# Optimization experiments

Hardware: AMD Instinct MI355X
Metric: run time of the kernel (lower is better)

## Reference

```python
import jax, jax.numpy as jnp
import numpy as np


def _scattering(image, mags, phases):
    # image: [B,S,S] real; mags/phases: [J,L,S,S] real (Fourier-domain Morlet filters)
    J = mags.shape[0]
    psi = (mags * jnp.exp(1j * phases)).astype(jnp.complex64)        # [J,L,S,S]
    xf = jnp.fft.fft2(image)                                          # [B,S,S] complex64
    # first-order: modulus of wavelet convolutions, all scales/orientations at once
    u1 = jnp.abs(jnp.fft.ifft2(xf[:, None, None] * psi[None]))        # [B,J,L,S,S]
    s0 = image.mean(axis=(-2, -1))                                    # [B]
    s1 = u1.mean(axis=(2, 3, 4))                                      # [B,J] (orientation-averaged)
    # second-order: only j2 > j1 (the nan-filtered entries in the original)
    s2_parts = []
    for j1 in range(J - 1):  # structural loop over scales, not data dims
        u1f = jnp.fft.fft2(u1[:, j1].astype(jnp.complex64))           # [B,L1,S,S]
        psi2 = psi[j1 + 1:]                                           # [J2,L2,S,S]
        v = jnp.abs(jnp.fft.ifft2(u1f[:, :, None, None] * psi2[None, None]))  # [B,L1,J2,L2,S,S]
        s2_parts.append(v.mean(axis=(1, 3, 4, 5)))                    # [B,J2]
    s2 = jnp.concatenate(s2_parts, axis=1)                            # [B, J*(J-1)/2]
    return s0, s1, s2


def setup_inputs() -> dict:
    key = jax.random.key(0)
    ks = jax.random.split(key, 8)
    B, S, J, L = 64, 128, 6, 4
    return {
        "image_batch": jax.random.normal(ks[0], (B, S, S), dtype=jnp.float32),
        "mags": jax.random.uniform(ks[1], (J, L, S, S), dtype=jnp.float32),
        "phases": jax.random.normal(ks[2], (J, L, S, S), dtype=jnp.float32),
        "w1": jax.random.normal(ks[3], (22, 16), dtype=jnp.float32) * 0.1,
        "b1": jnp.zeros((16,), dtype=jnp.float32),
        "w2": jax.random.normal(ks[4], (16, 16), dtype=jnp.float32) * 0.1,
        "b2": jnp.zeros((16,), dtype=jnp.float32),
        "w3": jax.random.normal(ks[5], (16, 1), dtype=jnp.float32) * 0.1,
        "b3": jnp.zeros((1,), dtype=jnp.float32),
    }


def reference(image_batch, mags, phases, w1, b1, w2, b2, w3, b3):
    s0, s1, s2 = _scattering(image_batch, mags, phases)
    x = jnp.concatenate([s0[:, None], s1, s2], axis=1)                # [B,22]
    x = jax.nn.relu(x @ w1 + b1)
    x = jax.nn.relu(x @ w2 + b2)
    x = jax.nn.sigmoid(x @ w3 + b3)
    return jnp.squeeze(x, axis=1)                                     # [B]
```

## Files before the change

kernel.cpp:

```cpp
#include <hip/hip_runtime.h>
#include <math.h>


#define SDIM 128
#define PLANE 16384
#define PITCH 129
#define NT 1024
#define TWO_PI 6.28318530717958647692f
#define PSIH_SCALE 16.0f

typedef _Float16 h2 __attribute__((ext_vector_type(2)));

constexpr float W16R[8] = {1.f, 0.9238795325f, 0.7071067812f, 0.3826834324f,
                           0.f, -0.3826834324f, -0.7071067812f, -0.9238795325f};
constexpr float W16I[8] = {0.f, -0.3826834324f, -0.7071067812f, -0.9238795325f,
                           -1.f, -0.9238795325f, -0.7071067812f, -0.3826834324f};

__device__ __forceinline__ float fast_sqrtf(float x) { return __builtin_amdgcn_sqrtf(x); }

__device__ __forceinline__ unsigned packbf(float re, float im) {
  const unsigned r = __float_as_uint(re) + 0x8000u;
  const unsigned i = __float_as_uint(im) + 0x8000u;
  return __builtin_amdgcn_perm(r, i, 0x07060302u);
}
__device__ __forceinline__ void unpackbf(unsigned u, float& re, float& im) {
  re = __uint_as_float(u & 0xFFFF0000u);
  im = __uint_as_float(u << 16);
}

union UHU { unsigned u; h2 h; };
__device__ __forceinline__ h2 u2h(unsigned u) { UHU x; x.u = u; return x.h; }
__device__ __forceinline__ unsigned h2u(h2 h) { UHU x; x.h = h; return x.u; }
__device__ __forceinline__ h2 bch2(float f) { const _Float16 h = (_Float16)f; h2 v = {h, h}; return v; }
__device__ __forceinline__ h2 mkh2(float a, float b) { h2 v = {(_Float16)a, (_Float16)b}; return v; }

__device__ __forceinline__ void stC(float2* s, int idx, float re, float im) { s[idx] = make_float2(re, im); }
__device__ __forceinline__ void ldC(const float2* s, int idx, float& re, float& im) { const float2 v = s[idx]; re = v.x; im = v.y; }
__device__ __forceinline__ void stC(unsigned* s, int idx, float re, float im) { s[idx] = packbf(re, im); }
__device__ __forceinline__ void ldC(const unsigned* s, int idx, float& re, float& im) { unpackbf(s[idx], re, im); }

__device__ __forceinline__ void load_tw(const float2* __restrict__ twg, int g,
                                        float* twr, float* twi) {
#pragma unroll
  for (int k = 1; k < 16; ++k) {
    const float2 w = twg[16 * g + k];
    twr[k] = __uint_as_float(__builtin_amdgcn_readfirstlane(__float_as_uint(w.x)));
    twi[k] = __uint_as_float(__builtin_amdgcn_readfirstlane(__float_as_uint(w.y)));
  }
}
__device__ __forceinline__ void load_twh(const uint2* __restrict__ twgh, int g,
                                         unsigned* twru, unsigned* twiu) {
#pragma unroll
  for (int k = 1; k < 16; ++k) {
    const uint2 w = twgh[16 * g + k];
    twru[k] = (unsigned)__builtin_amdgcn_readfirstlane((int)w.x);
    twiu[k] = (unsigned)__builtin_amdgcn_readfirstlane((int)w.y);
  }
}

template<bool INV>
__device__ __forceinline__ void bfly(float& ar, float& ai, float& br, float& bi, const int idx) {
  float tr, ti;
  if (idx == 0) { tr = br; ti = bi; }
  else if (idx == 4) {
    if (INV) { tr = -bi; ti = br; } else { tr = bi; ti = -br; }
  } else {
    const float wr = W16R[idx];
    const float wi = INV ? -W16I[idx] : W16I[idx];
    tr = br * wr - bi * wi;
    ti = br * wi + bi * wr;
  }
  br = ar - tr; bi = ai - ti;
  ar = ar + tr; ai = ai + ti;
}

#define CSWAP(re, im, a, b) { float _t = re[a]; re[a]=re[b]; re[b]=_t; _t = im[a]; im[a]=im[b]; im[b]=_t; }

template<bool INV>
__device__ __forceinline__ void dft16(float* re, float* im) {
  CSWAP(re, im, 1, 8) CSWAP(re, im, 2, 4) CSWAP(re, im, 3, 12)
  CSWAP(re, im, 5, 10) CSWAP(re, im, 7, 14) CSWAP(re, im, 11, 13)
#pragma unroll
  for (int ls = 1; ls <= 4; ++ls) {
    const int len = 1 << ls, half = len >> 1, tstep = 16 >> ls;
#pragma unroll
    for (int blk = 0; blk < 16; blk += len)
#pragma unroll
      for (int j = 0; j < half; ++j)
        bfly<INV>(re[blk + j], im[blk + j], re[blk + j + half], im[blk + j + half], j * tstep);
  }
}

template<bool INV>
__device__ __forceinline__ void dft8(float* re, float* im) {
  CSWAP(re, im, 1, 4) CSWAP(re, im, 3, 6)
#pragma unroll
  for (int ls = 1; ls <= 3; ++ls) {
    const int len = 1 << ls, half = len >> 1, tstep = 8 >> ls;
#pragma unroll
    for (int blk = 0; blk < 8; blk += len)
#pragma unroll
      for (int j = 0; j < half; ++j)
        bfly<INV>(re[blk + j], im[blk + j], re[blk + j + half], im[blk + j + half], j * tstep * 2);
  }
}

__device__ __forceinline__ void twmul_fwd(float* R, float* I, const float* twr, const float* twi) {
#pragma unroll
  for (int k = 1; k < 16; ++k) {
    const float r = R[k] * twr[k] - I[k] * twi[k];
    I[k] = R[k] * twi[k] + I[k] * twr[k]; R[k] = r;
  }
}
__device__ __forceinline__ void twmul_inv(float* R, float* I, const float* twr, const float* twi) {
#pragma unroll
  for (int k = 1; k < 16; ++k) {
    const float r = R[k] * twr[k] + I[k] * twi[k];
    I[k] = I[k] * twr[k] - R[k] * twi[k]; R[k] = r;
  }
}

template<typename S>
__device__ __forceinline__ void fwd_fft2(float* R, float* I, S* sC,
                                         int g, int q, const float* twr, const float* twi) {
  const int rb = q * PITCH;
  dft16<false>(R, I);
  twmul_fwd(R, I, twr, twi);
  __syncthreads();
#pragma unroll
  for (int k = 0; k < 16; ++k) stC(sC, rb + 8 * k + g, R[k], I[k]);
  __syncthreads();
#pragma unroll
  for (int t = 0; t < 8; ++t) {
    ldC(sC, rb + 16 * g + t, R[t], I[t]);
    ldC(sC, rb + 16 * g + 8 + t, R[8 + t], I[8 + t]);
  }
  dft8<false>(R, I); dft8<false>(R + 8, I + 8);
#pragma unroll
  for (int k2 = 0; k2 < 8; ++k2) {
    stC(sC, rb + 16 * g + k2, R[k2], I[k2]);
    stC(sC, rb + 16 * g + 8 + k2, R[8 + k2], I[8 + k2]);
  }
  __syncthreads();
#pragma unroll
  for (int m = 0; m < 16; ++m) ldC(sC, (g + 8 * m) * PITCH + q, R[m], I[m]);
  dft16<false>(R, I);
  twmul_fwd(R, I, twr, twi);
#pragma unroll
  for (int k = 0; k < 16; ++k) stC(sC, (8 * k + g) * PITCH + q, R[k], I[k]);
  __syncthreads();
#pragma unroll
  for (int u = 0; u < 8; ++u) {
    const int bp = (16 * g + 2 * u) * PITCH + q;
    ldC(sC, bp, R[2 * u], I[2 * u]);
    ldC(sC, bp + PITCH, R[2 * u + 1], I[2 * u + 1]);
  }
  dft8<false>(R, I); dft8<false>(R + 8, I + 8);
}

template<bool FIRST, typename S>
__device__ __forceinline__ void inv_fft2(float* R, float* I, S* sC,
                                         int g, int q, const float* twr, const float* twi) {
  const int rb = q * PITCH;
  dft8<true>(R, I); dft8<true>(R + 8, I + 8);
  if constexpr (!FIRST) __syncthreads();
#pragma unroll
  for (int t = 0; t < 16; ++t) stC(sC, rb + 16 * g + t, R[t], I[t]);
  __syncthreads();
#pragma unroll
  for (int k = 0; k < 16; ++k) ldC(sC, rb + 8 * k + g, R[k], I[k]);
  twmul_inv(R, I, twr, twi);
  dft16<true>(R, I);
#pragma unroll
  for (int m = 0; m < 16; ++m) stC(sC, rb + g + 8 * m, R[m], I[m]);
  __syncthreads();
#pragma unroll
  for (int u = 0; u < 8; ++u) {
    const int bp = (16 * g + 2 * u) * PITCH + q;
    ldC(sC, bp, R[2 * u], I[2 * u]);
    ldC(sC, bp + PITCH, R[2 * u + 1], I[2 * u + 1]);
  }
  dft8<true>(R, I); dft8<true>(R + 8, I + 8);
#pragma unroll
  for (int u = 0; u < 8; ++u) {
    const int bp = (16 * g + 2 * u) * PITCH + q;
    stC(sC, bp, R[2 * u], I[2 * u]);
    stC(sC, bp + PITCH, R[2 * u + 1], I[2 * u + 1]);
  }
  __syncthreads();
#pragma unroll
  for (int k = 0; k < 16; ++k) ldC(sC, (8 * k + g) * PITCH + q, R[k], I[k]);
  twmul_inv(R, I, twr, twi);
  dft16<true>(R, I);
}

__device__ __forceinline__ void bfly_h_inv(h2& ar, h2& ai, h2& br, h2& bi, const int idx) {
  h2 tr, ti;
  if (idx == 0) { tr = br; ti = bi; }
  else if (idx == 4) { tr = -bi; ti = br; }
  else {
    const h2 wr = bch2(W16R[idx]);
    const h2 wi = bch2(-W16I[idx]);
    tr = br * wr - bi * wi;
    ti = br * wi + bi * wr;
  }
  br = ar - tr; bi = ai - ti;
  ar = ar + tr; ai = ai + ti;
}

#define HSWAP(re, im, a, b) { h2 _t = re[a]; re[a]=re[b]; re[b]=_t; _t = im[a]; im[a]=im[b]; im[b]=_t; }

__device__ __forceinline__ void dft16h(h2* re, h2* im) {
  HSWAP(re, im, 1, 8) HSWAP(re, im, 2, 4) HSWAP(re, im, 3, 12)
  HSWAP(re, im, 5, 10) HSWAP(re, im, 7, 14) HSWAP(re, im, 11, 13)
#pragma unroll
  for (int ls = 1; ls <= 4; ++ls) {
    const int len = 1 << ls, half = len >> 1, tstep = 16 >> ls;
#pragma unroll
    for (int blk = 0; blk < 16; blk += len)
#pragma unroll
      for (int j = 0; j < half; ++j)
        bfly_h_inv(re[blk + j], im[blk + j], re[blk + j + half], im[blk + j + half], j * tstep);
  }
}

__device__ __forceinline__ void dft8h(h2* re, h2* im) {
  HSWAP(re, im, 1, 4) HSWAP(re, im, 3, 6)
#pragma unroll
  for (int ls = 1; ls <= 3; ++ls) {
    const int len = 1 << ls, half = len >> 1, tstep = 8 >> ls;
#pragma unroll
    for (int blk = 0; blk < 8; blk += len)
#pragma unroll
      for (int j = 0; j < half; ++j)
        bfly_h_inv(re[blk + j], im[blk + j], re[blk + j + half], im[blk + j + half], j * tstep * 2);
  }
}

__device__ __forceinline__ void twmul_inv_h(h2* R, h2* I, const unsigned* twru, const unsigned* twiu) {
#pragma unroll
  for (int k = 1; k < 16; ++k) {
    const h2 wr = u2h(twru[k]), wi = u2h(twiu[k]);
    const h2 r = R[k] * wr + I[k] * wi;
    I[k] = I[k] * wr - R[k] * wi;
    R[k] = r;
  }
}

template<int NW>
__device__ __forceinline__ float block_reduce_sum(float v, float* red, int tid) {
#pragma unroll
  for (int o = 32; o > 0; o >>= 1) v += __shfl_down(v, o);
  __syncthreads();
  if ((tid & 63) == 0) red[tid >> 6] = v;
  __syncthreads();
  float t = 0.0f;
  if (tid == 0) {
#pragma unroll
    for (int w = 0; w < NW; ++w) t += red[w];
  }
  return t;
}

__global__ __launch_bounds__(256) void k_psi(const float* __restrict__ mags,
                                             const float* __restrict__ phases,
                                             float2* __restrict__ psi,
                                             float2* __restrict__ twg,
                                             uint2* __restrict__ psih,
                                             uint2* __restrict__ twgh) {
  if (blockIdx.x == 0 && threadIdx.x < 128) {
    const int gg = threadIdx.x >> 4, k = threadIdx.x & 15;
    float sn, cs;
    __sincosf(-TWO_PI * (float)(gg * k) * (1.0f / 128.0f), &sn, &cs);
    twg[threadIdx.x] = make_float2(cs, sn);
    twgh[threadIdx.x] = make_uint2(h2u(bch2(cs)), h2u(bch2(sn)));
  }
  const int gid = blockIdx.x * 256 + threadIdx.x;
  if (gid < 24 * PLANE) {
    const int p = gid >> 14;
    const int rem = gid & (PLANE - 1);
    const int e = rem & 1;
    const int tt = (rem >> 1) & 1023;
    const int i = rem >> 11;
    const int j = 2 * i + e;
    const int g = tt >> 7, q = tt & 127;
    const int pr = 16 * g + j, pc = q;
    const int kr = (pr >> 3) + 16 * (pr & 7);
    const int kc = (pc >> 3) + 16 * (pc & 7);
    const int src = (p << 14) + kr * SDIM + kc;
    const float m = mags[src] * (1.0f / 16384.0f);
    float sn, cs;
    __sincosf(phases[src], &sn, &cs);
    psi[gid] = make_float2(m * cs, m * sn);
  } else if (gid < 24 * PLANE + 20 * 8192) {
    const int c = gid - 24 * PLANE;
    const int pidx = c >> 13;
    const int rem = c & 8191;
    const int j = rem >> 9;
    const int t512 = rem & 511;
    const int g = t512 >> 6, q = t512 & 63;
    const int row = 16 * g + j;
    const int plane = pidx + 4;
    const int kr = (row >> 3) + 16 * (row & 7);
    const int kc0 = (q >> 3) + 16 * (q & 7);
    const int q1 = q + 64;
    const int kc1 = (q1 >> 3) + 16 * (q1 & 7);
    const int src0 = (plane << 14) + kr * SDIM + kc0;
    const int src1 = (plane << 14) + kr * SDIM + kc1;
    const float scl = PSIH_SCALE / 16384.0f;
    const float m0 = mags[src0] * scl;
    const float m1 = mags[src1] * scl;
    float sn0, cs0, sn1, cs1;
    __sincosf(phases[src0], &sn0, &cs0);
    __sincosf(phases[src1], &sn1, &cs1);
    psih[c] = make_uint2(h2u(mkh2(m0 * cs0, m1 * cs1)), h2u(mkh2(m0 * sn0, m1 * sn1)));
  }
}

__global__ __launch_bounds__(NT) void k_img_fft(const float* __restrict__ img,
                                                float2* __restrict__ Xf,
                                                float* __restrict__ s0,
                                                const float2* __restrict__ twg) {
  __shared__ float2 sC[SDIM * PITCH];
  __shared__ float red[16];
  const int tid = threadIdx.x, b = blockIdx.x;
  const int g = __builtin_amdgcn_readfirstlane(tid >> 7);
  const int q = tid & 127;
  float twr[16], twi[16];
  load_tw(twg, g, twr, twi);
  const float* ip = img + b * PLANE;
  float sum = 0.0f;
#pragma unroll
  for (int kk = 0; kk < 16; ++kk) {
    const int e = tid + kk * NT;
    const float v = ip[e];
    sC[(e >> 7) * PITCH + (e & 127)] = make_float2(v, 0.0f);
    sum += v;
  }
  const float tot = block_reduce_sum<16>(sum, red, tid);
  if (tid == 0) s0[b] = tot * (1.0f / 16384.0f);
  __syncthreads();
  float R[16], I[16];
#pragma unroll
  for (int m = 0; m < 16; ++m) { R[m] = sC[q * PITCH + g + 8 * m].x; I[m] = 0.0f; }
  fwd_fft2(R, I, sC, g, q, twr, twi);
  float4* x4 = (float4*)Xf + (size_t)b * 8192 + tid;
#pragma unroll
  for (int i = 0; i < 8; ++i)
    x4[i * 1024] = make_float4(R[2 * i], I[2 * i], R[2 * i + 1], I[2 * i + 1]);
}

__global__ __launch_bounds__(NT) void k_scat_a(const float2* __restrict__ Xf,
                                               const float2* __restrict__ psi,
                                               float* __restrict__ s1num,
                                               unsigned* __restrict__ Ubuf,
                                               const float2* __restrict__ twg) {
  __shared__ unsigned sU[SDIM * PITCH];
  __shared__ float red[16];
  const int tid = threadIdx.x;
  const int g = __builtin_amdgcn_readfirstlane(tid >> 7);
  const int q = tid & 127;
  float twr[16], twi[16];
  load_tw(twg, g, twr, twi);
  const int bid = blockIdx.x;
  float R[16], I[16];

  if (bid < 1280) {
    const int j1 = bid >> 8;
    const int b = (bid & 255) >> 2;
    const int l1 = bid & 3;
    const float4* x4 = (const float4*)Xf + (size_t)b * 8192 + tid;
    const float4* p4 = (const float4*)psi + (size_t)(j1 * 4 + l1) * 8192 + tid;
#pragma unroll
    for (int i = 0; i < 8; ++i) {
      const float4 x = x4[i * 1024], v = p4[i * 1024];
      R[2 * i]     = x.x * v.x - x.y * v.y;  I[2 * i]     = x.x * v.y + x.y * v.x;
      R[2 * i + 1] = x.z * v.z - x.w * v.w;  I[2 * i + 1] = x.z * v.w + x.w * v.z;
    }
    inv_fft2<true>(R, I, sU, g, q, twr, twi);
    float s1sum = 0.0f;
#pragma unroll
    for (int m = 0; m < 16; ++m) {
      const float a = fast_sqrtf(R[m] * R[m] + I[m] * I[m]);
      s1sum += a; R[m] = a; I[m] = 0.0f;
    }
    fwd_fft2(R, I, sU, g, q, twr, twi);
    uint4 ob[4];
    unsigned* obs = (unsigned*)ob;
#pragma unroll
    for (int j = 0; j < 16; ++j) obs[j] = packbf(R[j], I[j]);
    uint4* o4 = (uint4*)Ubuf + (size_t)((b * 5 + j1) * 4 + l1) * 4096 + tid;
#pragma unroll
    for (int i = 0; i < 4; ++i) o4[i * 1024] = ob[i];
    const float tot = block_reduce_sum<16>(s1sum, red, tid);
    if (tid == 0) atomicAdd(&s1num[b * 6 + j1], tot);
  } else {
    const int idx = bid - 1280;
    const int b = idx >> 2, l = idx & 3;
    const float4* x4 = (const float4*)Xf + (size_t)b * 8192 + tid;
    const float4* p4 = (const float4*)psi + (size_t)(20 + l) * 8192 + tid;
#pragma unroll
    for (int i = 0; i < 8; ++i) {
      const float4 x = x4[i * 1024], v = p4[i * 1024];
      R[2 * i]     = x.x * v.x - x.y * v.y;  I[2 * i]     = x.x * v.y + x.y * v.x;
      R[2 * i + 1] = x.z * v.z - x.w * v.w;  I[2 * i + 1] = x.z * v.w + x.w * v.z;
    }
    inv_fft2<true>(R, I, sU, g, q, twr, twi);
    float s = 0.0f;
#pragma unroll
    for (int m = 0; m < 16; ++m) s += fast_sqrtf(R[m] * R[m] + I[m] * I[m]);
    const float tot = block_reduce_sum<16>(s, red, tid);
    if (tid == 0) atomicAdd(&s1num[b * 6 + 5], tot);
  }
}

__global__ __launch_bounds__(512, 4) void k_scat_b_rp(const uint2* __restrict__ psih,
                                                      const unsigned* __restrict__ Ubuf,
                                                      float* __restrict__ s2num,
                                                      const uint2* __restrict__ twgh) {
  __shared__ uint2 sU[64 * PITCH];
  __shared__ float red[8];
  const int tid = threadIdx.x;
  const int g = __builtin_amdgcn_readfirstlane(tid >> 6);
  const int q = tid & 63;
  unsigned twru[16], twiu[16];
  load_twh(twgh, g, twru, twiu);
  int t = blockIdx.x;
  const int l2 = t & 3; t >>= 2;
  const int pair = t % 15; t /= 15;
  const int l1 = t & 3;
  const int b = t >> 2;
  int j1 = 0, base = 0;
  if (pair >= 14)      { j1 = 4; base = 14; }
  else if (pair >= 12) { j1 = 3; base = 12; }
  else if (pair >= 9)  { j1 = 2; base = 9; }
  else if (pair >= 5)  { j1 = 1; base = 5; }
  const int j2 = j1 + 1 + (pair - base);
  const int pidx = j2 * 4 + l2 - 4;

  h2 R2[16], I2[16];
  {
    const uint4* u4 = (const uint4*)Ubuf + (size_t)((b * 5 + j1) * 4 + l1) * 4096;
    const int t0 = g * 128 + q;
    uint4 ua[4], ub[4];
#pragma unroll
    for (int i = 0; i < 4; ++i) { ua[i] = u4[i * 1024 + t0]; ub[i] = u4[i * 1024 + t0 + 64]; }
    const unsigned* uas = (const unsigned*)ua;
    const unsigned* ubs = (const unsigned*)ub;
    const uint2* ph = psih + (size_t)pidx * 8192 + tid;
#pragma unroll
    for (int j = 0; j < 16; ++j) {
      float urL, uiL, urH, uiH;
      unpackbf(uas[j], urL, uiL);
      unpackbf(ubs[j], urH, uiH);
      const h2 UR = mkh2(urL, urH), UI = mkh2(uiL, uiH);
      const uint2 pv = ph[j * 512];
      const h2 pr = u2h(pv.x), pi = u2h(pv.y);
      R2[j] = UR * pr - UI * pi;
      I2[j] = UR * pi + UI * pr;
    }
  }

  const int sb = q * PITCH;
  dft8h(R2, I2); dft8h(R2 + 8, I2 + 8);
#pragma unroll
  for (int s = 0; s < 16; ++s) sU[sb + 16 * g + s] = make_uint2(h2u(R2[s]), h2u(I2[s]));
  __syncthreads();
#pragma unroll
  for (int k = 0; k < 16; ++k) { const uint2 v = sU[sb + 8 * k + g]; R2[k] = u2h(v.x); I2[k] = u2h(v.y); }
  twmul_inv_h(R2, I2, twru, twiu);
  dft16h(R2, I2);
#pragma unroll
  for (int m = 0; m < 16; ++m) sU[sb + g + 8 * m] = make_uint2(h2u(R2[m]), h2u(I2[m]));
  __syncthreads();
  {
    const int s_base = (16 * g) & 63;
    const unsigned sel = (g < 4) ? 0x05040100u : 0x07060302u;
#pragma unroll
    for (int j = 0; j < 16; ++j) {
      const int cb = (s_base + j) * PITCH;
      const uint2 vA = sU[cb + q];
      const uint2 vB = sU[cb + q + 64];
      R2[j] = u2h(__builtin_amdgcn_perm(vB.x, vA.x, sel));
      I2[j] = u2h(__builtin_amdgcn_perm(vB.y, vA.y, sel));
    }
  }
  dft8h(R2, I2); dft8h(R2 + 8, I2 + 8);
  __syncthreads();
#pragma unroll
  for (int s = 0; s < 16; ++s) sU[sb + 16 * g + s] = make_uint2(h2u(R2[s]), h2u(I2[s]));
  __syncthreads();
#pragma unroll
  for (int k = 0; k < 16; ++k) { const uint2 v = sU[sb + 8 * k + g]; R2[k] = u2h(v.x); I2[k] = u2h(v.y); }
  twmul_inv_h(R2, I2, twru, twiu);
  dft16h(R2, I2);

  float vsum = 0.0f;
#pragma unroll
  for (int m = 0; m < 16; ++m) {
    const float rl = (float)R2[m].x, il = (float)I2[m].x;
    const float rh = (float)R2[m].y, ih = (float)I2[m].y;
    vsum += fast_sqrtf(rl * rl + il * il) + fast_sqrtf(rh * rh + ih * ih);
  }
  const float tot = block_reduce_sum<8>(vsum, red, tid);
  if (tid == 0) atomicAdd(&s2num[b * 15 + pair], tot);
}

__global__ __launch_bounds__(NT) void k_scat_b(const float2* __restrict__ psi,
                                               const unsigned* __restrict__ Ubuf,
                                               float* __restrict__ s2num,
                                               const float2* __restrict__ twg) {
  __shared__ unsigned sU[SDIM * PITCH];
  __shared__ float red[16];
  const int tid = threadIdx.x;
  const int g = __builtin_amdgcn_readfirstlane(tid >> 7);
  const int q = tid & 127;
  float twr[16], twi[16];
  load_tw(twg, g, twr, twi);
  int t = blockIdx.x;
  const int l2 = t & 3; t >>= 2;
  const int pair = t % 15; t /= 15;
  const int l1 = t & 3;
  const int b = t >> 2;
  int j1 = 0, base = 0;
  if (pair >= 14)      { j1 = 4; base = 14; }
  else if (pair >= 12) { j1 = 3; base = 12; }
  else if (pair >= 9)  { j1 = 2; base = 9; }
  else if (pair >= 5)  { j1 = 1; base = 5; }
  const int j2 = j1 + 1 + (pair - base);
  float R[16], I[16];
  {
    const uint4* u4 = (const uint4*)Ubuf + (size_t)((b * 5 + j1) * 4 + l1) * 4096 + tid;
    uint4 ub[4];
#pragma unroll
    for (int i = 0; i < 4; ++i) ub[i] = u4[i * 1024];
    const unsigned* ubs = (const unsigned*)ub;
    const float4* p4 = (const float4*)psi + (size_t)(j2 * 4 + l2) * 8192 + tid;
#pragma unroll
    for (int i = 0; i < 8; ++i) {
      const float4 v = p4[i * 1024];
      float ur, ui;
      unpackbf(ubs[2 * i], ur, ui);
      R[2 * i] = ur * v.x - ui * v.y;      I[2 * i] = ur * v.y + ui * v.x;
      unpackbf(ubs[2 * i + 1], ur, ui);
      R[2 * i + 1] = ur * v.z - ui * v.w;  I[2 * i + 1] = ur * v.w + ui * v.z;
    }
  }
  inv_fft2<true>(R, I, sU, g, q, twr, twi);
  float vsum = 0.0f;
#pragma unroll
  for (int m = 0; m < 16; ++m) vsum += fast_sqrtf(R[m] * R[m] + I[m] * I[m]);
  const float tot = block_reduce_sum<16>(vsum, red, tid);
  if (tid == 0) atomicAdd(&s2num[b * 15 + pair], tot);
}

__global__ __launch_bounds__(NT) void k_scat_mono(const float2* __restrict__ Xf,
                                                  const float2* __restrict__ psi,
                                                  float* __restrict__ s1num,
                                                  float* __restrict__ s2num,
                                                  const float2* __restrict__ twg) {
  __shared__ unsigned sU[SDIM * PITCH];
  __shared__ float red[16];
  const int tid = threadIdx.x;
  const int g = __builtin_amdgcn_readfirstlane(tid >> 7);
  const int q = tid & 127;
  float twr[16], twi[16];
  load_tw(twg, g, twr, twi);
  const int bid = blockIdx.x;
  float R[16], I[16];
  if (bid < 1280) {
    const int j1 = bid >> 8;
    const int b = (bid & 255) >> 2;
    const int l1 = bid & 3;
    const float4* x4 = (const float4*)Xf + (size_t)b * 8192 + tid;
    const float4* p4 = (const float4*)psi + (size_t)(j1 * 4 + l1) * 8192 + tid;
#pragma unroll
    for (int i = 0; i < 8; ++i) {
      const float4 x = x4[i * 1024], v = p4[i * 1024];
      R[2 * i]     = x.x * v.x - x.y * v.y;  I[2 * i]     = x.x * v.y + x.y * v.x;
      R[2 * i + 1] = x.z * v.z - x.w * v.w;  I[2 * i + 1] = x.z * v.w + x.w * v.z;
    }
    inv_fft2<true>(R, I, sU, g, q, twr, twi);
    float s1sum = 0.0f;
#pragma unroll
    for (int m = 0; m < 16; ++m) {
      const float a = fast_sqrtf(R[m] * R[m] + I[m] * I[m]);
      s1sum += a; R[m] = a; I[m] = 0.0f;
    }
    fwd_fft2(R, I, sU, g, q, twr, twi);
    float Ur[16], Ui[16];
#pragma unroll
    for (int k = 0; k < 16; ++k) { Ur[k] = R[k]; Ui[k] = I[k]; }
    {
      const float tot = block_reduce_sum<16>(s1sum, red, tid);
      if (tid == 0) atomicAdd(&s1num[b * 6 + j1], tot);
    }
    const int pb = (j1 * (11 - j1)) >> 1;
    int plane = (j1 + 1) * 4;
#pragma unroll 1
    for (int j2 = j1 + 1; j2 <= 5; ++j2) {
      float vsum = 0.0f;
#pragma unroll 1
      for (int l2 = 0; l2 < 4; ++l2) {
        const float4* q4 = (const float4*)psi + (size_t)plane * 8192 + tid;
#pragma unroll
        for (int i = 0; i < 8; ++i) {
          const float4 v = q4[i * 1024];
          R[2 * i]     = Ur[2 * i] * v.x - Ui[2 * i] * v.y;
          I[2 * i]     = Ur[2 * i] * v.y + Ui[2 * i] * v.x;
          R[2 * i + 1] = Ur[2 * i + 1] * v.z - Ui[2 * i + 1] * v.w;
          I[2 * i + 1] = Ur[2 * i + 1] * v.w + Ui[2 * i + 1] * v.z;
        }
        inv_fft2<false>(R, I, sU, g, q, twr, twi);
#pragma unroll
        for (int m = 0; m < 16; ++m) vsum += fast_sqrtf(R[m] * R[m] + I[m] * I[m]);
        ++plane;
      }
      const float tot = block_reduce_sum<16>(vsum, red, tid);
      if (tid == 0) atomicAdd(&s2num[b * 15 + pb + (j2 - j1 - 1)], tot);
    }
  } else {
    const int idx = bid - 1280;
    const int b = idx >> 2, l = idx & 3;
    const float4* x4 = (const float4*)Xf + (size_t)b * 8192 + tid;
    const float4* p4 = (const float4*)psi + (size_t)(20 + l) * 8192 + tid;
#pragma unroll
    for (int i = 0; i < 8; ++i) {
      const float4 x = x4[i * 1024], v = p4[i * 1024];
      R[2 * i]     = x.x * v.x - x.y * v.y;  I[2 * i]     = x.x * v.y + x.y * v.x;
      R[2 * i + 1] = x.z * v.z - x.w * v.w;  I[2 * i + 1] = x.z * v.w + x.w * v.z;
    }
    inv_fft2<true>(R, I, sU, g, q, twr, twi);
    float s = 0.0f;
#pragma unroll
    for (int m = 0; m < 16; ++m) s += fast_sqrtf(R[m] * R[m] + I[m] * I[m]);
    const float tot = block_reduce_sum<16>(s, red, tid);
    if (tid == 0) atomicAdd(&s1num[b * 6 + 5], tot);
  }
}

__global__ __launch_bounds__(64) void k_final(const float* __restrict__ s0,
                                              const float* __restrict__ s1num,
                                              const float* __restrict__ s2num,
                                              const float* __restrict__ w1,
                                              const float* __restrict__ b1,
                                              const float* __restrict__ w2,
                                              const float* __restrict__ b2,
                                              const float* __restrict__ w3,
                                              const float* __restrict__ b3,
                                              float* __restrict__ out,
                                              float s2scale) {
  const int b = threadIdx.x;
  if (b >= 64) return;
  float x[22];
  x[0] = s0[b];
#pragma unroll
  for (int j = 0; j < 6; ++j) x[1 + j] = s1num[b * 6 + j] * (1.0f / (4.0f * 16384.0f));
#pragma unroll
  for (int p = 0; p < 15; ++p) x[7 + p] = s2num[b * 15 + p] * s2scale;
  float h1[16];
#pragma unroll
  for (int o = 0; o < 16; ++o) {
    float t = b1[o];
    for (int i = 0; i < 22; ++i) t += x[i] * w1[i * 16 + o];
    h1[o] = fmaxf(t, 0.0f);
  }
  float h2a[16];
#pragma unroll
  for (int o = 0; o < 16; ++o) {
    float t = b2[o];
    for (int i = 0; i < 16; ++i) t += h1[i] * w2[i * 16 + o];
    h2a[o] = fmaxf(t, 0.0f);
  }
  float t = b3[0];
#pragma unroll
  for (int i = 0; i < 16; ++i) t += h2a[i] * w3[i];
  out[b] = 1.0f / (1.0f + expf(-t));
}

extern "C" void kernel_launch(void* const* d_in, const int* in_sizes, int n_in,
                              void* d_out, int out_size, void* d_ws, size_t ws_size,
                              hipStream_t stream) {
  (void)in_sizes; (void)n_in; (void)out_size;
  const float* image  = (const float*)d_in[0];
  const float* mags   = (const float*)d_in[1];
  const float* phases = (const float*)d_in[2];
  const float* w1 = (const float*)d_in[3];
  const float* b1 = (const float*)d_in[4];
  const float* w2 = (const float*)d_in[5];
  const float* b2 = (const float*)d_in[6];
  const float* w3 = (const float*)d_in[7];
  const float* b3 = (const float*)d_in[8];
  float* out = (float*)d_out;

  char* ws = (char*)d_ws;
  float2* psi = (float2*)ws;
  float2* Xf  = (float2*)(ws + 3145728);
  float*  s0  = (float*)(ws + 11534336);
  float*  s1n = s0 + 64;
  float*  s2n = s1n + 384;
  float2* twg = (float2*)(s2n + 960);
  uint2*  twgh = (uint2*)((char*)twg + 1024);
  unsigned* Ubuf = (unsigned*)(ws + 11542528);
  uint2*  psih = (uint2*)(ws + 95428608);
  const size_t need_r5 = 11542528ull + 83886080ull;
  const size_t need_h2 = need_r5 + 1310720ull;

  hipMemsetAsync(s1n, 0, (384 + 960) * sizeof(float), stream);
  if (ws_size >= need_h2) {
    k_psi<<<dim3(2176), dim3(256), 0, stream>>>(mags, phases, psi, twg, psih, twgh);
    k_img_fft<<<dim3(64), dim3(NT), 0, stream>>>(image, Xf, s0, twg);
    k_scat_a<<<dim3(1536), dim3(NT), 0, stream>>>(Xf, psi, s1n, Ubuf, twg);
    k_scat_b_rp<<<dim3(15360), dim3(512), 0, stream>>>(psih, Ubuf, s2n, twgh);
    k_final<<<dim3(1), dim3(64), 0, stream>>>(s0, s1n, s2n, w1, b1, w2, b2, w3, b3, out,
                                              1.0f / (16.0f * 16384.0f * PSIH_SCALE));
  } else if (ws_size >= need_r5) {
    k_psi<<<dim3(1536), dim3(256), 0, stream>>>(mags, phases, psi, twg, psih, twgh);
    k_img_fft<<<dim3(64), dim3(NT), 0, stream>>>(image, Xf, s0, twg);
    k_scat_a<<<dim3(1536), dim3(NT), 0, stream>>>(Xf, psi, s1n, Ubuf, twg);
    k_scat_b<<<dim3(15360), dim3(NT), 0, stream>>>(psi, Ubuf, s2n, twg);
    k_final<<<dim3(1), dim3(64), 0, stream>>>(s0, s1n, s2n, w1, b1, w2, b2, w3, b3, out,
                                              1.0f / (16.0f * 16384.0f));
  } else {
    k_psi<<<dim3(1536), dim3(256), 0, stream>>>(mags, phases, psi, twg, psih, twgh);
    k_img_fft<<<dim3(64), dim3(NT), 0, stream>>>(image, Xf, s0, twg);
    k_scat_mono<<<dim3(1536), dim3(NT), 0, stream>>>(Xf, psi, s1n, s2n, twg);
    k_final<<<dim3(1), dim3(64), 0, stream>>>(s0, s1n, s2n, w1, b1, w2, b2, w3, b3, out,
                                              1.0f / (16.0f * 16384.0f));
  }
}
```

Baseline: 463.7 us.

## Loop all second-order filters per block reusing loaded U plane

Restructures the second-order scattering kernel so that each block owns one (j1, b, l1) first-order plane and iterates over all j2/l2 filters. The U plane is loaded and unpacked once instead of once per filter, and the next filter's psi is prefetched into registers while the current FFT runs. Partial sums are reduced once per group of four orientations, so there are fewer atomics. The trade-off is far fewer blocks (1280 vs 15360) with imbalanced work across j1 (from 20 down to 4 iterations), which risks tail effects and lower occupancy.

```diff
diff --git a/kernel.cpp b/kernel.cpp
--- a/kernel.cpp
+++ b/kernel.cpp
@@ -245,6 +245,44 @@
     I[k] = I[k] * wr - R[k] * wi;
     R[k] = r;
   }
+}
+
+__device__ __forceinline__ void inv_rp_core(h2* R2, h2* I2, uint2* sU,
+                                            int g, int q,
+                                            const unsigned* twru, const unsigned* twiu) {
+  const int sb = q * PITCH;
+  dft8h(R2, I2); dft8h(R2 + 8, I2 + 8);
+#pragma unroll
+  for (int s = 0; s < 16; ++s) sU[sb + 16 * g + s] = make_uint2(h2u(R2[s]), h2u(I2[s]));
+  __syncthreads();
+#pragma unroll
+  for (int k = 0; k < 16; ++k) { const uint2 v = sU[sb + 8 * k + g]; R2[k] = u2h(v.x); I2[k] = u2h(v.y); }
+  twmul_inv_h(R2, I2, twru, twiu);
+  dft16h(R2, I2);
+#pragma unroll
+  for (int m = 0; m < 16; ++m) sU[sb + g + 8 * m] = make_uint2(h2u(R2[m]), h2u(I2[m]));
+  __syncthreads();
+  {
+    const int s_base = (16 * g) & 63;
+    const unsigned sel = (g < 4) ? 0x05040100u : 0x07060302u;
+#pragma unroll
+    for (int j = 0; j < 16; ++j) {
+      const int cb = (s_base + j) * PITCH;
+      const uint2 vA = sU[cb + q];
+      const uint2 vB = sU[cb + q + 64];
+      R2[j] = u2h(__builtin_amdgcn_perm(vB.x, vA.x, sel));
+      I2[j] = u2h(__builtin_amdgcn_perm(vB.y, vA.y, sel));
+    }
+  }
+  dft8h(R2, I2); dft8h(R2 + 8, I2 + 8);
+  __syncthreads();
+#pragma unroll
+  for (int s = 0; s < 16; ++s) sU[sb + 16 * g + s] = make_uint2(h2u(R2[s]), h2u(I2[s]));
+  __syncthreads();
+#pragma unroll
+  for (int k = 0; k < 16; ++k) { const uint2 v = sU[sb + 8 * k + g]; R2[k] = u2h(v.x); I2[k] = u2h(v.y); }
+  twmul_inv_h(R2, I2, twru, twiu);
+  dft16h(R2, I2);
 }
 
 template<int NW>
@@ -414,10 +452,10 @@
   }
 }
 
-__global__ __launch_bounds__(512, 4) void k_scat_b_rp(const uint2* __restrict__ psih,
-                                                      const unsigned* __restrict__ Ubuf,
-                                                      float* __restrict__ s2num,
-                                                      const uint2* __restrict__ twgh) {
+__global__ __launch_bounds__(512, 4) void k_scat_b_rpm(const uint2* __restrict__ psih,
+                                                       const unsigned* __restrict__ Ubuf,
+                                                       float* __restrict__ s2num,
+                                                       const uint2* __restrict__ twgh) {
   __shared__ uint2 sU[64 * PITCH];
   __shared__ float red[8];
   const int tid = threadIdx.x;
@@ -425,20 +463,14 @@
   const int q = tid & 63;
   unsigned twru[16], twiu[16];
   load_twh(twgh, g, twru, twiu);
-  int t = blockIdx.x;
-  const int l2 = t & 3; t >>= 2;
-  const int pair = t % 15; t /= 15;
-  const int l1 = t & 3;
-  const int b = t >> 2;
-  int j1 = 0, base = 0;
-  if (pair >= 14)      { j1 = 4; base = 14; }
-  else if (pair >= 12) { j1 = 3; base = 12; }
-  else if (pair >= 9)  { j1 = 2; base = 9; }
-  else if (pair >= 5)  { j1 = 1; base = 5; }
-  const int j2 = j1 + 1 + (pair - base);
-  const int pidx = j2 * 4 + l2 - 4;
-
-  h2 R2[16], I2[16];
+  const int bid = blockIdx.x;
+  const int j1 = bid >> 8;
+  const int b = (bid & 255) >> 2;
+  const int l1 = bid & 3;
+  const int pb = (j1 * (11 - j1)) >> 1;
+  const int nit = (5 - j1) * 4;
+
+  h2 UR2[16], UI2[16];
   {
     const uint4* u4 = (const uint4*)Ubuf + (size_t)((b * 5 + j1) * 4 + l1) * 4096;
     const int t0 = g * 128 + q;
@@ -447,63 +479,51 @@
     for (int i = 0; i < 4; ++i) { ua[i] = u4[i * 1024 + t0]; ub[i] = u4[i * 1024 + t0 + 64]; }
     const unsigned* uas = (const unsigned*)ua;
     const unsigned* ubs = (const unsigned*)ub;
-    const uint2* ph = psih + (size_t)pidx * 8192 + tid;
 #pragma unroll
     for (int j = 0; j < 16; ++j) {
       float urL, uiL, urH, uiH;
       unpackbf(uas[j], urL, uiL);
       unpackbf(ubs[j], urH, uiH);
-      const h2 UR = mkh2(urL, urH), UI = mkh2(uiL, uiH);
-      const uint2 pv = ph[j * 512];
-      const h2 pr = u2h(pv.x), pi = u2h(pv.y);
-      R2[j] = UR * pr - UI * pi;
-      I2[j] = UR * pi + UI * pr;
-    }
-  }
-
-  const int sb = q * PITCH;
-  dft8h(R2, I2); dft8h(R2 + 8, I2 + 8);
-#pragma unroll
-  for (int s = 0; s < 16; ++s) sU[sb + 16 * g + s] = make_uint2(h2u(R2[s]), h2u(I2[s]));
-  __syncthreads();
-#pragma unroll
-  for (int k = 0; k < 16; ++k) { const uint2 v = sU[sb + 8 * k + g]; R2[k] = u2h(v.x); I2[k] = u2h(v.y); }
-  twmul_inv_h(R2, I2, twru, twiu);
-  dft16h(R2, I2);
-#pragma unroll
-  for (int m = 0; m < 16; ++m) sU[sb + g + 8 * m] = make_uint2(h2u(R2[m]), h2u(I2[m]));
-  __syncthreads();
+      UR2[j] = mkh2(urL, urH);
+      UI2[j] = mkh2(uiL, uiH);
+    }
+  }
+
+  uint2 buf[16];
   {
-    const int s_base = (16 * g) & 63;
-    const unsigned sel = (g < 4) ? 0x05040100u : 0x07060302u;
+    const uint2* ph = psih + (size_t)(4 * j1) * 8192 + tid;
+#pragma unroll
+    for (int j = 0; j < 16; ++j) buf[j] = ph[j * 512];
+  }
+
+  float vsum = 0.0f;
+  for (int it = 0; it < nit; ++it) {
+    h2 R2[16], I2[16];
 #pragma unroll
     for (int j = 0; j < 16; ++j) {
-      const int cb = (s_base + j) * PITCH;
-      const uint2 vA = sU[cb + q];
-      const uint2 vB = sU[cb + q + 64];
-      R2[j] = u2h(__builtin_amdgcn_perm(vB.x, vA.x, sel));
-      I2[j] = u2h(__builtin_amdgcn_perm(vB.y, vA.y, sel));
-    }
-  }
-  dft8h(R2, I2); dft8h(R2 + 8, I2 + 8);
-  __syncthreads();
-#pragma unroll
-  for (int s = 0; s < 16; ++s) sU[sb + 16 * g + s] = make_uint2(h2u(R2[s]), h2u(I2[s]));
-  __syncthreads();
-#pragma unroll
-  for (int k = 0; k < 16; ++k) { const uint2 v = sU[sb + 8 * k + g]; R2[k] = u2h(v.x); I2[k] = u2h(v.y); }
-  twmul_inv_h(R2, I2, twru, twiu);
-  dft16h(R2, I2);
-
-  float vsum = 0.0f;
-#pragma unroll
-  for (int m = 0; m < 16; ++m) {
-    const float rl = (float)R2[m].x, il = (float)I2[m].x;
-    const float rh = (float)R2[m].y, ih = (float)I2[m].y;
-    vsum += fast_sqrtf(rl * rl + il * il) + fast_sqrtf(rh * rh + ih * ih);
-  }
-  const float tot = block_reduce_sum<8>(vsum, red, tid);
-  if (tid == 0) atomicAdd(&s2num[b * 15 + pair], tot);
+      const h2 pr = u2h(buf[j].x), pi = u2h(buf[j].y);
+      R2[j] = UR2[j] * pr - UI2[j] * pi;
+      I2[j] = UR2[j] * pi + UI2[j] * pr;
+    }
+    if (it + 1 < nit) {
+      const uint2* phn = psih + (size_t)(4 * j1 + it + 1) * 8192 + tid;
+#pragma unroll
+      for (int j = 0; j < 16; ++j) buf[j] = phn[j * 512];
+    }
+    if (it) __syncthreads();
+    inv_rp_core(R2, I2, sU, g, q, twru, twiu);
+#pragma unroll
+    for (int m = 0; m < 16; ++m) {
+      const float rl = (float)R2[m].x, il = (float)I2[m].x;
+      const float rh = (float)R2[m].y, ih = (float)I2[m].y;
+      vsum += fast_sqrtf(rl * rl + il * il) + fast_sqrtf(rh * rh + ih * ih);
+    }
+    if ((it & 3) == 3) {
+      const float tot = block_reduce_sum<8>(vsum, red, tid);
+      if (tid == 0) atomicAdd(&s2num[b * 15 + pb + (it >> 2)], tot);
+      vsum = 0.0f;
+    }
+  }
 }
 
 __global__ __launch_bounds__(NT) void k_scat_b(const float2* __restrict__ psi,
@@ -711,7 +731,7 @@
     k_psi<<<dim3(2176), dim3(256), 0, stream>>>(mags, phases, psi, twg, psih, twgh);
     k_img_fft<<<dim3(64), dim3(NT), 0, stream>>>(image, Xf, s0, twg);
     k_scat_a<<<dim3(1536), dim3(NT), 0, stream>>>(Xf, psi, s1n, Ubuf, twg);
-    k_scat_b_rp<<<dim3(15360), dim3(512), 0, stream>>>(psih, Ubuf, s2n, twgh);
+    k_scat_b_rpm<<<dim3(1280), dim3(512), 0, stream>>>(psih, Ubuf, s2n, twgh);
     k_final<<<dim3(1), dim3(64), 0, stream>>>(s0, s1n, s2n, w1, b1, w2, b2, w3, b3, out,
                                               1.0f / (16.0f * 16384.0f * PSIH_SCALE));
   } else if (ws_size >= need_r5) {
```

After: 446.8 us. -3.7%, faster.
